# Performance work log

Hardware: AMD Instinct MI355X
Metric: run time of the kernel (lower is better)

The kernel has to match this reference:

```python
import jax, jax.numpy as jnp
import numpy as np

D_MODEL = 1024
N_HEADS = 16
D_HEAD = D_MODEL // N_HEADS
SCALE = D_HEAD ** 0.5
EPS_NORM = 1e-10
EPS_CLAMP = 1e-06


def _sphere(x):
    # project to unit sphere along last dim
    n = jnp.maximum(jnp.linalg.norm(x, axis=-1, keepdims=True), EPS_NORM)
    return x / n


def setup_inputs() -> dict:
    key = jax.random.key(0)
    ks = jax.random.split(key, 9)
    s = 1.0 / np.sqrt(D_MODEL)  # torch Linear default init scale
    inp = {
        "H": jax.random.normal(ks[0], (2, 2048, D_MODEL), dtype=jnp.float32),
        "W_q": jax.random.uniform(ks[1], (D_MODEL, D_MODEL), jnp.float32, -s, s),
        "b_q": jax.random.uniform(ks[2], (D_MODEL,), jnp.float32, -s, s),
        "W_k": jax.random.uniform(ks[3], (D_MODEL, D_MODEL), jnp.float32, -s, s),
        "b_k": jax.random.uniform(ks[4], (D_MODEL,), jnp.float32, -s, s),
        "W_v": jax.random.uniform(ks[5], (D_MODEL, D_MODEL), jnp.float32, -s, s),
        "b_v": jax.random.uniform(ks[6], (D_MODEL,), jnp.float32, -s, s),
        "W_o": jax.random.uniform(ks[7], (D_MODEL, D_MODEL), jnp.float32, -s, s),
        "b_o": jax.random.uniform(ks[8], (D_MODEL,), jnp.float32, -s, s),
    }
    return inp


def reference(H, W_q, b_q, W_k, b_k, W_v, b_v, W_o, b_o):
    B, S, _ = H.shape
    # torch Linear: y = x @ W.T + b
    def proj(W, b):
        y = jnp.einsum('bsd,ed->bse', H, W) + b
        return _sphere(y.reshape(B, S, N_HEADS, D_HEAD).transpose(0, 2, 1, 3))  # [B,H,S,Dh]
    Q = proj(W_q, b_q)
    K = proj(W_k, b_k)
    V = proj(W_v, b_v)
    cos = jnp.einsum('bhqd,bhkd->bhqk', Q, K)
    cos = jnp.clip(cos, -1.0 + EPS_CLAMP, 1.0 - EPS_CLAMP)
    scores = -jnp.arccos(cos) / SCALE
    attn = jax.nn.softmax(scores, axis=-1)
    out = jnp.einsum('bhqk,bhkd->bhqd', attn, V)
    out = out.transpose(0, 2, 1, 3).reshape(B, S, D_MODEL)
    return jnp.einsum('bsd,ed->bse', out, W_o) + b_o
```

## Files before the change

### kernel.cpp

```cpp
#include <hip/hip_runtime.h>
#include <hip/hip_bf16.h>

typedef __bf16 bf16_t;
typedef __bf16 bf16x8 __attribute__((ext_vector_type(8)));
typedef __bf16 bf16x4 __attribute__((ext_vector_type(4)));
typedef float f32x2 __attribute__((ext_vector_type(2)));
typedef float f32x4 __attribute__((ext_vector_type(4)));
typedef float f32x16 __attribute__((ext_vector_type(16)));

#define NB 2
#define SEQ 2048
#define DMODEL 1024
#define NHEAD 16
#define DHEAD 64

__device__ inline void gload_lds16(const void* g, void* lds) {
  __builtin_amdgcn_global_load_lds((const __attribute__((address_space(1))) void*)g,
                                   (__attribute__((address_space(3))) void*)lds,
                                   16, 0, 0);
}

__global__ __launch_bounds__(256) void cvt_all_kernel(
    const float* __restrict__ H,  const float* __restrict__ Wq, const float* __restrict__ Wk,
    const float* __restrict__ Wv, const float* __restrict__ Wo,
    bf16_t* __restrict__ Hb, bf16_t* __restrict__ Wqb, bf16_t* __restrict__ Wkb,
    bf16_t* __restrict__ Wvb, bf16_t* __restrict__ Wob)
{
  const int b = blockIdx.x;
  const float* src; bf16_t* dst; int idx;
  if (b < 4096) { src = H; dst = Hb; idx = b; }
  else {
    const int r = b - 4096; const int s = r >> 10; idx = r & 1023;
    src = (s == 0) ? Wq : (s == 1) ? Wk : (s == 2) ? Wv : Wo;
    dst = (s == 0) ? Wqb : (s == 1) ? Wkb : (s == 2) ? Wvb : Wob;
  }
  const int i = idx * 256 + threadIdx.x;
  float4 v = ((const float4*)src)[i];
  bf16x4 o;
  o[0] = (bf16_t)v.x; o[1] = (bf16_t)v.y; o[2] = (bf16_t)v.z; o[3] = (bf16_t)v.w;
  ((bf16x4*)dst)[i] = o;
}

template<int MODE>
__global__ __launch_bounds__(256) void gemm_bt_kernel(
    const bf16_t* __restrict__ A,
    const bf16_t* __restrict__ W0, const bf16_t* __restrict__ W1, const bf16_t* __restrict__ W2,
    const float* __restrict__ bias0, const float* __restrict__ bias1, const float* __restrict__ bias2,
    void* out0, void* out1, void* out2)
{
  __shared__ bf16_t As[128 * 64];
  __shared__ bf16_t Bs[128 * 64];
  const int tid = threadIdx.x;
  const int lane = tid & 63;
  const int w = tid >> 6;
  const int mt = blockIdx.y, nt = blockIdx.x, z = blockIdx.z;
  const bf16_t* Wp = (z == 0) ? W0 : ((z == 1) ? W1 : W2);
  const float* bp  = (z == 0) ? bias0 : ((z == 1) ? bias1 : bias2);

  const int wr = w >> 1, wc = w & 1;
  const int fr = lane & 15, fq = lane >> 4;

  const int r_in = lane >> 3;
  const int cswz = ((lane & 7) ^ (r_in & 7)) << 4;
  const unsigned lbase = (unsigned)__builtin_amdgcn_readfirstlane(w * 4096);

  f32x4 acc[4][4] = {};

  const char* Ab = (const char*)(A + (size_t)mt * 128 * DMODEL);
  const char* Bb = (const char*)(Wp + (size_t)nt * 128 * DMODEL);

  for (int kt = 0; kt < DMODEL / 64; ++kt) {
    const size_t k0b = (size_t)kt * 128;
    #pragma unroll
    for (int i = 0; i < 4; ++i) {
      const size_t row = (size_t)(w * 32 + i * 8 + r_in);
      gload_lds16(Ab + row * (DMODEL * 2) + k0b + cswz, (char*)As + lbase + i * 1024);
      gload_lds16(Bb + row * (DMODEL * 2) + k0b + cswz, (char*)Bs + lbase + i * 1024);
    }
    __syncthreads();

    bf16x8 a[4][2], b[4][2];
    #pragma unroll
    for (int m = 0; m < 4; ++m)
      #pragma unroll
      for (int ks = 0; ks < 2; ++ks)
        a[m][ks] = *(const bf16x8*)((const char*)As + (wr * 64 + m * 16 + fr) * 128 +
                                    ((ks * 64 + fq * 16) ^ ((fr & 7) << 4)));
    #pragma unroll
    for (int n = 0; n < 4; ++n)
      #pragma unroll
      for (int ks = 0; ks < 2; ++ks)
        b[n][ks] = *(const bf16x8*)((const char*)Bs + (wc * 64 + n * 16 + fr) * 128 +
                                    ((ks * 64 + fq * 16) ^ ((fr & 7) << 4)));
    __builtin_amdgcn_s_setprio(1);
    #pragma unroll
    for (int m = 0; m < 4; ++m)
      #pragma unroll
      for (int n = 0; n < 4; ++n)
        #pragma unroll
        for (int ks = 0; ks < 2; ++ks)
          acc[m][n] = __builtin_amdgcn_mfma_f32_16x16x32_bf16(a[m][ks], b[n][ks], acc[m][n], 0, 0, 0);
    __builtin_amdgcn_s_setprio(0);
    __syncthreads();
  }

  float bv[4];
  const int cb = nt * 128 + wc * 64;
  #pragma unroll
  for (int n = 0; n < 4; ++n) bv[n] = bp[cb + n * 16 + fr];

  if constexpr (MODE == 0) {
    float* outp = (float*)out0;
    #pragma unroll
    for (int m = 0; m < 4; ++m) {
      #pragma unroll
      for (int j = 0; j < 4; ++j) {
        const int row = mt * 128 + wr * 64 + m * 16 + fq * 4 + j;
        float* orow = outp + (size_t)row * DMODEL + cb;
        #pragma unroll
        for (int n = 0; n < 4; ++n)
          orow[n * 16 + fr] = acc[m][n][j] + bv[n];
      }
    }
  } else {
    const int h = nt * 2 + wc;
    #pragma unroll
    for (int m = 0; m < 4; ++m) {
      #pragma unroll
      for (int j = 0; j < 4; ++j) {
        float v0 = acc[m][0][j] + bv[0];
        float v1 = acc[m][1][j] + bv[1];
        float v2 = acc[m][2][j] + bv[2];
        float v3 = acc[m][3][j] + bv[3];
        float ss = v0 * v0 + v1 * v1 + v2 * v2 + v3 * v3;
        ss += __shfl_xor(ss, 1);
        ss += __shfl_xor(ss, 2);
        ss += __shfl_xor(ss, 4);
        ss += __shfl_xor(ss, 8);
        const float inv = 1.0f / fmaxf(sqrtf(ss), 1e-10f);
        const int row = mt * 128 + wr * 64 + m * 16 + fq * 4 + j;
        const int bb = row >> 11, sr = row & (SEQ - 1);
        if (z < 2) {
          bf16_t* op = ((z == 0) ? (bf16_t*)out0 : (bf16_t*)out1)
                       + (((size_t)(bb * NHEAD + h)) * SEQ + sr) * DHEAD;
          op[0 * 16 + fr] = (bf16_t)(v0 * inv);
          op[1 * 16 + fr] = (bf16_t)(v1 * inv);
          op[2 * 16 + fr] = (bf16_t)(v2 * inv);
          op[3 * 16 + fr] = (bf16_t)(v3 * inv);
        } else {
          bf16_t* vp = (bf16_t*)out2 + ((size_t)(bb * NHEAD + h)) * DHEAD * SEQ + sr;
          vp[(size_t)(0 * 16 + fr) * SEQ] = (bf16_t)(v0 * inv);
          vp[(size_t)(1 * 16 + fr) * SEQ] = (bf16_t)(v1 * inv);
          vp[(size_t)(2 * 16 + fr) * SEQ] = (bf16_t)(v2 * inv);
          vp[(size_t)(3 * 16 + fr) * SEQ] = (bf16_t)(v3 * inv);
        }
      }
    }
  }
}

#define PSWAP(x, y) asm("v_permlane32_swap_b32 %0, %1" : "+v"(x), "+v"(y))
#define CVTPK(d, a, b) asm("v_cvt_pk_bf16_f32 %0, %1, %2" : "=v"(d) : "v"(a), "v"(b))
#define WAITVM(n) asm volatile("s_waitcnt vmcnt(" #n ")" ::: "memory")
#define V2(x) ((f32x2){(x), (x)})

__device__ inline void score_pack(const f32x16& accp, float& l_acc, bf16x8& pf0, bf16x8& pf1) {
  f32x2 p2[8];
  #pragma unroll
  for (int i = 0; i < 8; ++i) {
    f32x2 cv; cv[0] = accp[2 * i]; cv[1] = accp[2 * i + 1];
    const f32x2 c2 = cv * cv;
    f32x2 a = __builtin_elementwise_fma(c2, V2(0.00379774f), V2(0.00558036f));
    a = __builtin_elementwise_fma(c2, a, V2(0.00937500f));
    a = __builtin_elementwise_fma(c2, a, V2(0.02083333f));
    a = __builtin_elementwise_fma(c2, a, V2(0.12500000f));
    const f32x2 s = a * cv;
    f32x2 e = __builtin_elementwise_fma(s, V2(0.16666667f), V2(0.5f));
    e = __builtin_elementwise_fma(s, e, V2(1.0f));
    e = __builtin_elementwise_fma(s, e, V2(1.0f));
    p2[i] = e;
  }
  const f32x2 t01 = p2[0] + p2[1], t23 = p2[2] + p2[3];
  const f32x2 t45 = p2[4] + p2[5], t67 = p2[6] + p2[7];
  const f32x2 tt = (t01 + t23) + (t45 + t67);
  l_acc += tt[0] + tt[1];
  unsigned dwA0, dwA1, dwA2, dwA3, dwB0, dwB1, dwB2, dwB3;
  CVTPK(dwA0, p2[0][0], p2[0][1]);  CVTPK(dwB0, p2[1][0], p2[1][1]);
  CVTPK(dwA1, p2[2][0], p2[2][1]);  CVTPK(dwB1, p2[3][0], p2[3][1]);
  CVTPK(dwA2, p2[4][0], p2[4][1]);  CVTPK(dwB2, p2[5][0], p2[5][1]);
  CVTPK(dwA3, p2[6][0], p2[6][1]);  CVTPK(dwB3, p2[7][0], p2[7][1]);
  PSWAP(dwA0, dwA1);  PSWAP(dwB0, dwB1);
  PSWAP(dwA2, dwA3);  PSWAP(dwB2, dwB3);
  typedef unsigned u32x4_ __attribute__((ext_vector_type(4)));
  u32x4_ t0_ = { dwA0, dwB0, dwA1, dwB1 };
  u32x4_ t1_ = { dwA2, dwB2, dwA3, dwB3 };
  pf0 = __builtin_bit_cast(bf16x8, t0_);
  pf1 = __builtin_bit_cast(bf16x8, t1_);
}

template<int KS>
__global__ __launch_bounds__(256, 3) void mfma_attn_kernel(
    const bf16_t* __restrict__ Qb, const bf16_t* __restrict__ Kb,
    const bf16_t* __restrict__ Vt, bf16_t* __restrict__ Oat,
    float* __restrict__ o_part, float* __restrict__ l_part)
{
  __shared__ char smem[32768];

  const int tid = threadIdx.x;
  const int lane = tid & 63;
  const int qw = tid >> 6;
  const int l31 = lane & 31, l5 = lane >> 5;

  const int p = blockIdx.x;
  const int xcd = p & 7;
  const int j = p >> 3;
  int bh, qt, z;
  if (KS == 2) { bh = xcd * 4 + (j >> 5); qt = (j & 31) >> 1; z = j & 1; }
  else         { bh = xcd * 4 + (j >> 4); qt = j & 15;        z = 0;     }
  const int q0 = qt * 128 + qw * 32;
  const int NT = (KS == 2) ? 16 : 32;

  const bf16_t* Qp = Qb + ((size_t)bh * SEQ + q0 + l31) * DHEAD + l5 * 8;
  bf16x8 b_q[4];
  #pragma unroll
  for (int m = 0; m < 4; ++m)
    b_q[m] = *(const bf16x8*)(Qp + m * 16);

  const char* KbaseH = (const char*)(Kb + (size_t)bh * SEQ * DHEAD) + (size_t)z * 1024 * DHEAD * 2;
  const char* VbaseH = (const char*)(Vt + (size_t)bh * DHEAD * SEQ) + (size_t)z * 1024 * 2;

  const int chA = 2 * qw, chB = 2 * qw + 1;
  int koffA, koffB, voffA, voffB;
  {
    const int rA = chA * 4 + (lane >> 4), rB = chB * 4 + (lane >> 4);
    const int c = (lane & 15) * 16;
    const int cpA = c ^ ((rA & 15) << 4), cpB = c ^ ((rB & 15) << 4);
    koffA = (rA + ((cpA >> 7) << 5)) * 128 + (cpA & 127);
    koffB = (rB + ((cpB >> 7) << 5)) * 128 + (cpB & 127);
    voffA = (rA + ((cpA >> 7) << 5)) * (SEQ * 2) + (cpA & 127);
    voffB = (rB + ((cpB >> 7) << 5)) * (SEQ * 2) + (cpB & 127);
  }
  const unsigned stKA = (unsigned)__builtin_amdgcn_readfirstlane(chA * 1024);
  const unsigned stKB = (unsigned)__builtin_amdgcn_readfirstlane(chB * 1024);

  const int swz = (l31 & 15) << 4;
  const unsigned kRow = l31 * 256;

  f32x16 acc_o0 = {}, acc_o1 = {};
  float l_acc = 0.0f;

  #define STAGE(t, buf)                                                                    \
    do {                                                                                   \
      const char* Kt_ = KbaseH + (size_t)(t) * 8192;                                       \
      const char* Vc_ = VbaseH + (size_t)(t) * 128;                                        \
      gload_lds16(Kt_ + koffA, smem + stKA + (buf) * 16384);                               \
      gload_lds16(Kt_ + koffB, smem + stKB + (buf) * 16384);                               \
      gload_lds16(Vc_ + voffA, smem + stKA + (buf) * 16384 + 8192);                        \
      gload_lds16(Vc_ + voffB, smem + stKB + (buf) * 16384 + 8192);                        \
    } while (0)

  #define CHUNK(buf, c0)                                                                   \
    do {                                                                                   \
      const char* kb_ = smem + (buf) * 16384 + kRow;                                       \
      bf16x8 ak0 = *(const bf16x8*)(kb_ + (((c0) * 128 +  0 + l5 * 16) ^ swz));            \
      bf16x8 ak1 = *(const bf16x8*)(kb_ + (((c0) * 128 + 32 + l5 * 16) ^ swz));            \
      bf16x8 ak2 = *(const bf16x8*)(kb_ + (((c0) * 128 + 64 + l5 * 16) ^ swz));            \
      bf16x8 ak3 = *(const bf16x8*)(kb_ + (((c0) * 128 + 96 + l5 * 16) ^ swz));            \
      f32x16 accp = {};                                                                    \
      __builtin_amdgcn_s_setprio(1);                                                       \
      accp = __builtin_amdgcn_mfma_f32_32x32x16_bf16(ak0, b_q[0], accp, 0, 0, 0);          \
      accp = __builtin_amdgcn_mfma_f32_32x32x16_bf16(ak1, b_q[1], accp, 0, 0, 0);          \
      accp = __builtin_amdgcn_mfma_f32_32x32x16_bf16(ak2, b_q[2], accp, 0, 0, 0);          \
      accp = __builtin_amdgcn_mfma_f32_32x32x16_bf16(ak3, b_q[3], accp, 0, 0, 0);          \
      __builtin_amdgcn_s_setprio(0);                                                       \
      const char* vb_ = smem + (buf) * 16384 + 8192 + kRow;                                \
      bf16x8 av00 = *(const bf16x8*)(vb_ + ((      (c0) * 64 +  0 + l5 * 16) ^ swz));      \
      bf16x8 av01 = *(const bf16x8*)(vb_ + ((      (c0) * 64 + 32 + l5 * 16) ^ swz));      \
      bf16x8 av10 = *(const bf16x8*)(vb_ + ((128 + (c0) * 64 +  0 + l5 * 16) ^ swz));      \
      bf16x8 av11 = *(const bf16x8*)(vb_ + ((128 + (c0) * 64 + 32 + l5 * 16) ^ swz));      \
      bf16x8 pf0, pf1;                                                                     \
      score_pack(accp, l_acc, pf0, pf1);                                                   \
      __builtin_amdgcn_s_setprio(1);                                                       \
      acc_o0 = __builtin_amdgcn_mfma_f32_32x32x16_bf16(av00, pf0, acc_o0, 0, 0, 0);        \
      acc_o0 = __builtin_amdgcn_mfma_f32_32x32x16_bf16(av01, pf1, acc_o0, 0, 0, 0);        \
      acc_o1 = __builtin_amdgcn_mfma_f32_32x32x16_bf16(av10, pf0, acc_o1, 0, 0, 0);        \
      acc_o1 = __builtin_amdgcn_mfma_f32_32x32x16_bf16(av11, pf1, acc_o1, 0, 0, 0);        \
      __builtin_amdgcn_s_setprio(0);                                                       \
    } while (0)

  #define TILE(buf) do { CHUNK(buf, 0); CHUNK(buf, 1); } while (0)

  STAGE(0, 0);
  STAGE(1, 1);

  for (int t2 = 0; t2 < NT / 2 - 1; ++t2) {
    WAITVM(4);
    __builtin_amdgcn_s_barrier();
    TILE(0);
    __builtin_amdgcn_s_barrier();
    STAGE(2 * t2 + 2, 0);
    WAITVM(4);
    __builtin_amdgcn_s_barrier();
    TILE(1);
    __builtin_amdgcn_s_barrier();
    STAGE(2 * t2 + 3, 1);
  }
  WAITVM(4);
  __builtin_amdgcn_s_barrier();
  TILE(0);
  WAITVM(0);
  __builtin_amdgcn_s_barrier();
  TILE(1);
  #undef TILE
  #undef CHUNK
  #undef STAGE

  l_acc += __shfl_xor(l_acc, 32);

  if (KS == 2) {
    float* po = o_part + ((size_t)z * (32 * SEQ) + (size_t)bh * SEQ + q0 + l31) * 64;
    #pragma unroll
    for (int blk = 0; blk < 2; ++blk) {
      const f32x16& ao = blk ? acc_o1 : acc_o0;
      #pragma unroll
      for (int g = 0; g < 4; ++g) {
        f32x4 ov = { ao[4 * g + 0], ao[4 * g + 1], ao[4 * g + 2], ao[4 * g + 3] };
        *(f32x4*)(po + blk * 32 + 8 * g + 4 * l5) = ov;
      }
    }
    if (lane < 32)
      l_part[(size_t)z * (32 * SEQ) + (size_t)bh * SEQ + q0 + l31] = l_acc;
  } else {
    const float invl = __builtin_amdgcn_rcpf(l_acc);
    const int bb = bh >> 4, h = bh & 15;
    bf16_t* op = Oat + ((size_t)bb * SEQ + q0 + l31) * DMODEL + h * DHEAD;
    #pragma unroll
    for (int blk = 0; blk < 2; ++blk) {
      const f32x16& ao = blk ? acc_o1 : acc_o0;
      #pragma unroll
      for (int g = 0; g < 4; ++g) {
        bf16x4 ov;
        ov[0] = (bf16_t)(ao[4 * g + 0] * invl);
        ov[1] = (bf16_t)(ao[4 * g + 1] * invl);
        ov[2] = (bf16_t)(ao[4 * g + 2] * invl);
        ov[3] = (bf16_t)(ao[4 * g + 3] * invl);
        *(bf16x4*)(op + blk * 32 + 8 * g + 4 * l5) = ov;
      }
    }
  }
}

__global__ __launch_bounds__(256) void attn_combine_kernel(
    const float* __restrict__ o_part, const float* __restrict__ l_part,
    bf16_t* __restrict__ Oat)
{
  const int idx = blockIdx.x * 256 + threadIdx.x;
  const int row = idx >> 4, u = idx & 15;
  const float l = l_part[row] + l_part[32 * SEQ + row];
  const float inv = __builtin_amdgcn_rcpf(l);
  const f32x4 a = ((const f32x4*)o_part)[idx];
  const f32x4 b = ((const f32x4*)o_part)[(32 * SEQ * 16) + idx];
  bf16x4 o;
  o[0] = (bf16_t)((a[0] + b[0]) * inv);
  o[1] = (bf16_t)((a[1] + b[1]) * inv);
  o[2] = (bf16_t)((a[2] + b[2]) * inv);
  o[3] = (bf16_t)((a[3] + b[3]) * inv);
  const int bh = row >> 11, q = row & (SEQ - 1);
  const int bb = bh >> 4, h = bh & 15;
  ((bf16x4*)(Oat + ((size_t)bb * SEQ + q) * DMODEL + h * DHEAD))[u] = o;
}

extern "C" void kernel_launch(void* const* d_in, const int* in_sizes, int n_in,
                              void* d_out, int out_size, void* d_ws, size_t ws_size,
                              hipStream_t stream)
{
  const float* H  = (const float*)d_in[0];
  const float* Wq = (const float*)d_in[1];
  const float* bq = (const float*)d_in[2];
  const float* Wk = (const float*)d_in[3];
  const float* bk = (const float*)d_in[4];
  const float* Wv = (const float*)d_in[5];
  const float* bv = (const float*)d_in[6];
  const float* Wo = (const float*)d_in[7];
  const float* bo = (const float*)d_in[8];
  float* out = (float*)d_out;

  char* ws = (char*)d_ws;
  bf16_t* Hb  = (bf16_t*)(ws);
  bf16_t* Wqb = (bf16_t*)(ws + (8u << 20));
  bf16_t* Wkb = (bf16_t*)(ws + (10u << 20));
  bf16_t* Wvb = (bf16_t*)(ws + (12u << 20));
  bf16_t* Wob = (bf16_t*)(ws + (14u << 20));
  bf16_t* Qbf = (bf16_t*)(ws + (16u << 20));
  bf16_t* Kbf = (bf16_t*)(ws + (24u << 20));
  bf16_t* Vtb = (bf16_t*)(ws + (32u << 20));
  bf16_t* Oat = (bf16_t*)(ws + (40u << 20));
  float*  o_part = (float*)(ws + (48u << 20));
  float*  l_part = (float*)(ws + (80u << 20));
  const bool ks2 = ws_size >= ((80ull << 20) + 524288ull);

  cvt_all_kernel<<<8192, 256, 0, stream>>>(H, Wq, Wk, Wv, Wo, Hb, Wqb, Wkb, Wvb, Wob);

  gemm_bt_kernel<1><<<dim3(8, 32, 3), 256, 0, stream>>>(
      Hb, Wqb, Wkb, Wvb, bq, bk, bv, Qbf, Kbf, Vtb);

  if (ks2) {
    mfma_attn_kernel<2><<<1024, 256, 0, stream>>>(Qbf, Kbf, Vtb, Oat, o_part, l_part);
    attn_combine_kernel<<<4096, 256, 0, stream>>>(o_part, l_part, Oat);
  } else {
    mfma_attn_kernel<1><<<512, 256, 0, stream>>>(Qbf, Kbf, Vtb, Oat, o_part, l_part);
  }

  gemm_bt_kernel<0><<<dim3(8, 32, 1), 256, 0, stream>>>(
      Oat, Wob, Wob, Wob, bo, bo, bo, out, out, out);
}
```

Baseline: 144.8 us.

## Merge split-K attention halves into one workgroup with LDS reduction

```diff
diff --git a/kernel.cpp b/kernel.cpp
--- a/kernel.cpp
+++ b/kernel.cpp
@@ -198,27 +198,25 @@
   pf1 = __builtin_bit_cast(bf16x8, t1_);
 }
 
-template<int KS>
-__global__ __launch_bounds__(256, 3) void mfma_attn_kernel(
+__global__ __launch_bounds__(512, 2) void mfma_attn_kernel(
     const bf16_t* __restrict__ Qb, const bf16_t* __restrict__ Kb,
-    const bf16_t* __restrict__ Vt, bf16_t* __restrict__ Oat,
-    float* __restrict__ o_part, float* __restrict__ l_part)
+    const bf16_t* __restrict__ Vt, bf16_t* __restrict__ Oat)
 {
-  __shared__ char smem[32768];
+  __shared__ char smem[65536];
 
   const int tid = threadIdx.x;
   const int lane = tid & 63;
-  const int qw = tid >> 6;
+  const int w = tid >> 6;
+  const int qw = w & 3, kh = w >> 2;
   const int l31 = lane & 31, l5 = lane >> 5;
 
   const int p = blockIdx.x;
   const int xcd = p & 7;
   const int j = p >> 3;
-  int bh, qt, z;
-  if (KS == 2) { bh = xcd * 4 + (j >> 5); qt = (j & 31) >> 1; z = j & 1; }
-  else         { bh = xcd * 4 + (j >> 4); qt = j & 15;        z = 0;     }
+  const int bh = xcd * 4 + (j >> 4);
+  const int qt = j & 15;
   const int q0 = qt * 128 + qw * 32;
-  const int NT = (KS == 2) ? 16 : 32;
+  const int NT = 16;
 
   const bf16_t* Qp = Qb + ((size_t)bh * SEQ + q0 + l31) * DHEAD + l5 * 8;
   bf16x8 b_q[4];
@@ -226,8 +224,8 @@
   for (int m = 0; m < 4; ++m)
     b_q[m] = *(const bf16x8*)(Qp + m * 16);
 
-  const char* KbaseH = (const char*)(Kb + (size_t)bh * SEQ * DHEAD) + (size_t)z * 1024 * DHEAD * 2;
-  const char* VbaseH = (const char*)(Vt + (size_t)bh * DHEAD * SEQ) + (size_t)z * 1024 * 2;
+  const char* KbaseH = (const char*)(Kb + (size_t)bh * SEQ * DHEAD) + (size_t)kh * 1024 * DHEAD * 2;
+  const char* VbaseH = (const char*)(Vt + (size_t)bh * DHEAD * SEQ) + (size_t)kh * 1024 * 2;
 
   const int chA = 2 * qw, chB = 2 * qw + 1;
   int koffA, koffB, voffA, voffB;
@@ -240,8 +238,9 @@
     voffA = (rA + ((cpA >> 7) << 5)) * (SEQ * 2) + (cpA & 127);
     voffB = (rB + ((cpB >> 7) << 5)) * (SEQ * 2) + (cpB & 127);
   }
-  const unsigned stKA = (unsigned)__builtin_amdgcn_readfirstlane(chA * 1024);
-  const unsigned stKB = (unsigned)__builtin_amdgcn_readfirstlane(chB * 1024);
+  const unsigned stKA = (unsigned)__builtin_amdgcn_readfirstlane(kh * 32768 + chA * 1024);
+  const unsigned stKB = (unsigned)__builtin_amdgcn_readfirstlane(kh * 32768 + chB * 1024);
+  const unsigned rb0  = (unsigned)__builtin_amdgcn_readfirstlane(kh * 32768);
 
   const int swz = (l31 & 15) << 4;
   const unsigned kRow = l31 * 256;
@@ -261,7 +260,7 @@
 
   #define CHUNK(buf, c0)                                                                   \
     do {                                                                                   \
-      const char* kb_ = smem + (buf) * 16384 + kRow;                                       \
+      const char* kb_ = smem + rb0 + (buf) * 16384 + kRow;                                 \
       bf16x8 ak0 = *(const bf16x8*)(kb_ + (((c0) * 128 +  0 + l5 * 16) ^ swz));            \
       bf16x8 ak1 = *(const bf16x8*)(kb_ + (((c0) * 128 + 32 + l5 * 16) ^ swz));            \
       bf16x8 ak2 = *(const bf16x8*)(kb_ + (((c0) * 128 + 64 + l5 * 16) ^ swz));            \
@@ -273,7 +272,7 @@
       accp = __builtin_amdgcn_mfma_f32_32x32x16_bf16(ak2, b_q[2], accp, 0, 0, 0);          \
       accp = __builtin_amdgcn_mfma_f32_32x32x16_bf16(ak3, b_q[3], accp, 0, 0, 0);          \
       __builtin_amdgcn_s_setprio(0);                                                       \
-      const char* vb_ = smem + (buf) * 16384 + 8192 + kRow;                                \
+      const char* vb_ = smem + rb0 + (buf) * 16384 + 8192 + kRow;                          \
       bf16x8 av00 = *(const bf16x8*)(vb_ + ((      (c0) * 64 +  0 + l5 * 16) ^ swz));      \
       bf16x8 av01 = *(const bf16x8*)(vb_ + ((      (c0) * 64 + 32 + l5 * 16) ^ swz));      \
       bf16x8 av10 = *(const bf16x8*)(vb_ + ((128 + (c0) * 64 +  0 + l5 * 16) ^ swz));      \
@@ -317,20 +316,25 @@
 
   l_acc += __shfl_xor(l_acc, 32);
 
-  if (KS == 2) {
-    float* po = o_part + ((size_t)z * (32 * SEQ) + (size_t)bh * SEQ + q0 + l31) * 64;
-    #pragma unroll
-    for (int blk = 0; blk < 2; ++blk) {
-      const f32x16& ao = blk ? acc_o1 : acc_o0;
-      #pragma unroll
-      for (int g = 0; g < 4; ++g) {
-        f32x4 ov = { ao[4 * g + 0], ao[4 * g + 1], ao[4 * g + 2], ao[4 * g + 3] };
-        *(f32x4*)(po + blk * 32 + 8 * g + 4 * l5) = ov;
-      }
-    }
-    if (lane < 32)
-      l_part[(size_t)z * (32 * SEQ) + (size_t)bh * SEQ + q0 + l31] = l_acc;
-  } else {
+  __syncthreads();
+  float* cO = (float*)smem;
+  float* cL = (float*)(smem + 32768);
+  if (kh == 1) {
+    #pragma unroll
+    for (int r = 0; r < 16; ++r) {
+      cO[(qw * 32 + r) * 64 + lane] = acc_o0[r];
+      cO[(qw * 32 + 16 + r) * 64 + lane] = acc_o1[r];
+    }
+    cL[qw * 64 + lane] = l_acc;
+  }
+  __syncthreads();
+  if (kh == 0) {
+    #pragma unroll
+    for (int r = 0; r < 16; ++r) {
+      acc_o0[r] += cO[(qw * 32 + r) * 64 + lane];
+      acc_o1[r] += cO[(qw * 32 + 16 + r) * 64 + lane];
+    }
+    l_acc += cL[qw * 64 + lane];
     const float invl = __builtin_amdgcn_rcpf(l_acc);
     const int bb = bh >> 4, h = bh & 15;
     bf16_t* op = Oat + ((size_t)bb * SEQ + q0 + l31) * DMODEL + h * DHEAD;
@@ -348,26 +352,6 @@
       }
     }
   }
-}
-
-__global__ __launch_bounds__(256) void attn_combine_kernel(
-    const float* __restrict__ o_part, const float* __restrict__ l_part,
-    bf16_t* __restrict__ Oat)
-{
-  const int idx = blockIdx.x * 256 + threadIdx.x;
-  const int row = idx >> 4, u = idx & 15;
-  const float l = l_part[row] + l_part[32 * SEQ + row];
-  const float inv = __builtin_amdgcn_rcpf(l);
-  const f32x4 a = ((const f32x4*)o_part)[idx];
-  const f32x4 b = ((const f32x4*)o_part)[(32 * SEQ * 16) + idx];
-  bf16x4 o;
-  o[0] = (bf16_t)((a[0] + b[0]) * inv);
-  o[1] = (bf16_t)((a[1] + b[1]) * inv);
-  o[2] = (bf16_t)((a[2] + b[2]) * inv);
-  o[3] = (bf16_t)((a[3] + b[3]) * inv);
-  const int bh = row >> 11, q = row & (SEQ - 1);
-  const int bb = bh >> 4, h = bh & 15;
-  ((bf16x4*)(Oat + ((size_t)bb * SEQ + q) * DMODEL + h * DHEAD))[u] = o;
 }
 
 extern "C" void kernel_launch(void* const* d_in, const int* in_sizes, int n_in,
@@ -395,21 +379,13 @@
   bf16_t* Kbf = (bf16_t*)(ws + (24u << 20));
   bf16_t* Vtb = (bf16_t*)(ws + (32u << 20));
   bf16_t* Oat = (bf16_t*)(ws + (40u << 20));
-  float*  o_part = (float*)(ws + (48u << 20));
-  float*  l_part = (float*)(ws + (80u << 20));
-  const bool ks2 = ws_size >= ((80ull << 20) + 524288ull);
 
   cvt_all_kernel<<<8192, 256, 0, stream>>>(H, Wq, Wk, Wv, Wo, Hb, Wqb, Wkb, Wvb, Wob);
 
   gemm_bt_kernel<1><<<dim3(8, 32, 3), 256, 0, stream>>>(
       Hb, Wqb, Wkb, Wvb, bq, bk, bv, Qbf, Kbf, Vtb);
 
-  if (ks2) {
-    mfma_attn_kernel<2><<<1024, 256, 0, stream>>>(Qbf, Kbf, Vtb, Oat, o_part, l_part);
-    attn_combine_kernel<<<4096, 256, 0, stream>>>(o_part, l_part, Oat);
-  } else {
-    mfma_attn_kernel<1><<<512, 256, 0, stream>>>(Qbf, Kbf, Vtb, Oat, o_part, l_part);
-  }
+  mfma_attn_kernel<<<512, 512, 0, stream>>>(Qbf, Kbf, Vtb, Oat);
 
   gemm_bt_kernel<0><<<dim3(8, 32, 1), 256, 0, stream>>>(
       Oat, Wob, Wob, Wob, bo, bo, bo, out, out, out);
```

New measurement: 140.5 us. -3.0%, faster.
